# Kernel optimization log

Hardware: AMD Instinct MI355X
Metric: run time of the kernel (lower is better)

Reference implementation:

```python
import jax, jax.numpy as jnp
import numpy as np

HEADS = 16
DIM_HEAD = 64
SCALE = DIM_HEAD ** -0.5


def setup_inputs() -> dict:
    key = jax.random.key(0)
    k1, k2, k3, k4 = jax.random.split(key, 4)
    dim = 1024
    inner = HEADS * DIM_HEAD  # 1024
    b, n = 4, 2048
    x = jax.random.normal(k1, (b, n, dim), dtype=jnp.float32)
    # weights stored as [in, out] (equivalent math to torch Linear)
    w_qkv = jax.random.normal(k2, (dim, inner * 3), dtype=jnp.float32) * (dim ** -0.5)
    w_out = jax.random.normal(k3, (inner, dim), dtype=jnp.float32) * (inner ** -0.5)
    b_out = jax.random.normal(k4, (dim,), dtype=jnp.float32) * 0.01
    return {"x": x, "w_qkv": w_qkv, "w_out": w_out, "b_out": b_out}


def reference(x, w_qkv, w_out, b_out):
    b, n, dim = x.shape
    qkv = x @ w_qkv                                   # [b, n, 3*inner]
    q, k, v = jnp.split(qkv, 3, axis=-1)
    def to_heads(t):
        return t.reshape(b, n, HEADS, DIM_HEAD).transpose(0, 2, 1, 3)  # b h n d
    q, k, v = to_heads(q) * SCALE, to_heads(k), to_heads(v)
    dots = jnp.einsum('bhid,bhjd->bhij', q, k)        # [b, h, n, n]
    mask_value = -jnp.finfo(dots.dtype).max
    causal_mask = jnp.triu(jnp.ones((n, n), dtype=bool), k=1)
    dots = jnp.where(causal_mask, mask_value, dots)
    attn = jax.nn.softmax(dots, axis=-1)
    out = jnp.einsum('bhij,bhjd->bhid', attn, v)      # [b, h, n, d]
    out = out.transpose(0, 2, 1, 3).reshape(b, n, HEADS * DIM_HEAD)
    return out @ w_out + b_out
```

## Files before the change

### kernel.cpp

```cpp
#include <hip/hip_runtime.h>
#include <hip/hip_bf16.h>
#include <stdint.h>

typedef __attribute__((ext_vector_type(8))) short bf16x8;
typedef __attribute__((ext_vector_type(4))) float f32x4;
typedef __attribute__((ext_vector_type(4))) unsigned int uint32x4;

#define TOKENS 8192
#define DMODEL 1024
#define NQKV   3072
#define NSEQ   2048
#define NHEAD  16
#define DHEAD  64

__device__ __forceinline__ ushort f32_bf16(float f) {
    uint32_t u = __builtin_bit_cast(uint32_t, f);
    u = (u + 0x7fffu + ((u >> 16) & 1u)) >> 16;
    return (ushort)u;
}

__device__ __forceinline__ unsigned int cvt_pk_bf16(float lo, float hi) {
    unsigned int r;
    asm("v_cvt_pk_bf16_f32 %0, %1, %2" : "=v"(r) : "v"(lo), "v"(hi));
    return r;
}
__device__ __forceinline__ void permlane32_swap(unsigned int& a, unsigned int& b) {
    asm("v_permlane32_swap_b32 %0, %1" : "+v"(a), "+v"(b));
}
__device__ __forceinline__ void permlane16_swap(unsigned int& a, unsigned int& b) {
    asm("v_permlane16_swap_b32 %0, %1" : "+v"(a), "+v"(b));
}
__device__ __forceinline__ unsigned opaque_copy(unsigned x) {
    unsigned y;
    asm("v_mov_b32 %0, %1" : "=v"(y) : "v"(x));
    return y;
}

__device__ __forceinline__ float red_max_g(float x) {
    unsigned a = __builtin_bit_cast(unsigned, x);
    unsigned b = opaque_copy(a);
    permlane16_swap(a, b);
    float r = fmaxf(__builtin_bit_cast(float, a), __builtin_bit_cast(float, b));
    unsigned c = __builtin_bit_cast(unsigned, r);
    unsigned d = opaque_copy(c);
    permlane32_swap(c, d);
    return fmaxf(__builtin_bit_cast(float, c), __builtin_bit_cast(float, d));
}
__device__ __forceinline__ float red_sum_g(float x) {
    unsigned a = __builtin_bit_cast(unsigned, x);
    unsigned b = opaque_copy(a);
    permlane16_swap(a, b);
    float r = __builtin_bit_cast(float, a) + __builtin_bit_cast(float, b);
    unsigned c = __builtin_bit_cast(unsigned, r);
    unsigned d = opaque_copy(c);
    permlane32_swap(c, d);
    return __builtin_bit_cast(float, c) + __builtin_bit_cast(float, d);
}

__device__ __forceinline__ void gload16(const void* g, void* l) {
    __builtin_amdgcn_global_load_lds(
        (const __attribute__((address_space(1))) void*)g,
        (__attribute__((address_space(3))) void*)l, 16, 0, 0);
}

__global__ void cvt_x_kernel(const float* __restrict__ x, ushort* __restrict__ xb) {
    int i = blockIdx.x * 256 + threadIdx.x;
    float4 v = reinterpret_cast<const float4*>(x)[i];
    ushort4 o;
    o.x = f32_bf16(v.x); o.y = f32_bf16(v.y);
    o.z = f32_bf16(v.z); o.w = f32_bf16(v.w);
    reinterpret_cast<ushort4*>(xb)[i] = o;
}

__global__ __launch_bounds__(256) void cvt_wt_kernel(
    const float* __restrict__ w, ushort* __restrict__ wt, int N)
{
    __shared__ float tile[64][65];
    const int tid = threadIdx.x;
    const int r  = tid >> 4;
    const int c4 = (tid & 15) * 4;
    const int n0 = blockIdx.x * 64;
    const int k0 = blockIdx.y * 64;
    #pragma unroll
    for (int i = 0; i < 4; ++i) {
        const float4 v = *reinterpret_cast<const float4*>(&w[(size_t)(k0 + r + i * 16) * N + n0 + c4]);
        tile[r + i * 16][c4 + 0] = v.x;
        tile[r + i * 16][c4 + 1] = v.y;
        tile[r + i * 16][c4 + 2] = v.z;
        tile[r + i * 16][c4 + 3] = v.w;
    }
    __syncthreads();
    #pragma unroll
    for (int i = 0; i < 4; ++i) {
        ushort4 o;
        o.x = f32_bf16(tile[c4 + 0][r + i * 16]);
        o.y = f32_bf16(tile[c4 + 1][r + i * 16]);
        o.z = f32_bf16(tile[c4 + 2][r + i * 16]);
        o.w = f32_bf16(tile[c4 + 3][r + i * 16]);
        *reinterpret_cast<ushort4*>(&wt[(size_t)(n0 + r + i * 16) * 1024 + k0 + c4]) = o;
    }
}

__device__ __forceinline__ void barf() {
    asm volatile("" ::: "memory");
    __builtin_amdgcn_s_barrier();
    asm volatile("" ::: "memory");
}

template<int MODE>
__global__ __launch_bounds__(256) void gemm_bt(
    const ushort* __restrict__ A, const ushort* __restrict__ Bt,
    ushort* __restrict__ Qb, ushort* __restrict__ Kb, ushort* __restrict__ Vtb,
    float* __restrict__ Out, const float* __restrict__ bias)
{
    constexpr int K = 1024;
    __shared__ __align__(16) ushort As[2][128 * 32];
    __shared__ __align__(16) ushort Bs[2][128 * 32];

    const int lane = threadIdx.x & 63;
    const int w    = threadIdx.x >> 6;
    const int l16  = lane & 15;
    const int g    = lane >> 4;
    const int row0 = blockIdx.y * 128;
    const int col0 = blockIdx.x * 128;
    const int wr   = (w >> 1) * 64;
    const int wc   = (w & 1) * 64;

    const int srow  = w * 16 + (lane >> 2);
    const int sswz8 = ((lane & 3) ^ ((lane >> 3) & 3)) * 8;
    const ushort* Ag = A  + (size_t)(row0 + srow) * K + sswz8;
    const ushort* Bg = Bt + (size_t)(col0 + srow) * K + sswz8;
    const int woff = w * (16 * 32);

    const int cq8 = (g ^ ((l16 >> 1) & 3)) * 8;

    f32x4 acc[4][4] = {};

#define GSTAGE(BUF, KK) do {                                             \
        gload16(Ag + (KK),          &As[BUF][woff]);                     \
        gload16(Ag + 64 * K + (KK), &As[BUF][woff + 64 * 32]);           \
        gload16(Bg + (KK),          &Bs[BUF][woff]);                     \
        gload16(Bg + 64 * K + (KK), &Bs[BUF][woff + 64 * 32]);           \
    } while (0)

#define GCOMPUTE(BUF) do {                                               \
        bf16x8 a[4], b[4];                                               \
        _Pragma("unroll")                                                \
        for (int m = 0; m < 4; ++m)                                      \
            a[m] = *reinterpret_cast<const bf16x8*>(                     \
                &As[BUF][(wr + m * 16 + l16) * 32 + cq8]);               \
        _Pragma("unroll")                                                \
        for (int n = 0; n < 4; ++n)                                      \
            b[n] = *reinterpret_cast<const bf16x8*>(                     \
                &Bs[BUF][(wc + n * 16 + l16) * 32 + cq8]);               \
        _Pragma("unroll")                                                \
        for (int m = 0; m < 4; ++m)                                      \
            _Pragma("unroll")                                            \
            for (int n = 0; n < 4; ++n)                                  \
                acc[m][n] = __builtin_amdgcn_mfma_f32_16x16x32_bf16(     \
                    a[m], b[n], acc[m][n], 0, 0, 0);                     \
    } while (0)

    GSTAGE(0, 0);
    GSTAGE(1, 32);
    for (int kk = 0; kk + 128 <= K; kk += 64) {
        asm volatile("s_waitcnt vmcnt(4)" ::: "memory");
        barf();
        GCOMPUTE(0);
        barf();
        GSTAGE(0, kk + 64);
        asm volatile("s_waitcnt vmcnt(4)" ::: "memory");
        barf();
        GCOMPUTE(1);
        barf();
        GSTAGE(1, kk + 96);
    }
    asm volatile("s_waitcnt vmcnt(4)" ::: "memory");
    barf();
    GCOMPUTE(0);
    asm volatile("s_waitcnt vmcnt(0)" ::: "memory");
    barf();
    GCOMPUTE(1);
#undef GSTAGE
#undef GCOMPUTE

    if (MODE == 0) {
        const int part = col0 >> 10;
        const float QSC = 0.18033688011112042f;
        #pragma unroll
        for (int m = 0; m < 4; ++m) {
            const int trow = row0 + wr + m * 16 + 4 * g;
            #pragma unroll
            for (int n = 0; n < 4; ++n) {
                const int c  = col0 + wc + n * 16 + l16;
                const int cc = c & 1023;
                const int h  = cc >> 6, d = cc & 63;
                #pragma unroll
                for (int jj = 0; jj < 4; ++jj) {
                    const int t  = trow + jj;
                    const int bb = t >> 11, nn = t & 2047;
                    const float v = acc[m][n][jj];
                    const size_t bhid = (size_t)(bb * NHEAD + h);
                    if (part == 0)
                        Qb[(bhid * NSEQ + nn) * DHEAD + d] = f32_bf16(v * QSC);
                    else if (part == 1)
                        Kb[(bhid * NSEQ + nn) * DHEAD + d] = f32_bf16(v);
                    else
                        Vtb[bhid * (NSEQ * DHEAD) + (size_t)(nn >> 5) * (DHEAD * 32)
                            + d * 32 + (nn & 31)] = f32_bf16(v);
                }
            }
        }
    } else {
        #pragma unroll
        for (int m = 0; m < 4; ++m) {
            const int trow = row0 + wr + m * 16 + 4 * g;
            #pragma unroll
            for (int n = 0; n < 4; ++n) {
                const int c = col0 + wc + n * 16 + l16;
                const float bv = bias[c];
                #pragma unroll
                for (int jj = 0; jj < 4; ++jj)
                    Out[(size_t)(trow + jj) * DMODEL + c] = acc[m][n][jj] + bv;
            }
        }
    }
}

__device__ __forceinline__ void attn_qk(
    int kt, int qr0s, int l16, int g,
    const bf16x8 (&kk)[4][2],
    const bf16x8 qf0, const bf16x8 qf1,
    f32x4 (&oacc)[4], float& mrun, float& lsum,
    bf16x8& pf0, bf16x8& pf1)
{
    const f32x4 zero = {};
    f32x4 s[4];
    __builtin_amdgcn_s_setprio(1);
    #pragma unroll
    for (int t = 0; t < 4; ++t) {
        s[t] = __builtin_amdgcn_mfma_f32_16x16x32_bf16(kk[t][0], qf0, zero, 0, 0, 0);
        s[t] = __builtin_amdgcn_mfma_f32_16x16x32_bf16(kk[t][1], qf1, s[t], 0, 0, 0);
    }
    __builtin_amdgcn_s_setprio(0);
    if (kt + 63 > qr0s) {
        const int kb = kt + 4 * g - (qr0s + l16);
        #pragma unroll
        for (int t = 0; t < 4; ++t)
            #pragma unroll
            for (int jj = 0; jj < 4; ++jj)
                if (kb + 16 * t + jj > 0) s[t][jj] = -1e30f;
    }
    const float m0 = fmaxf(fmaxf(s[0][0], s[0][1]), s[0][2]);
    const float m1 = fmaxf(fmaxf(s[0][3], s[1][0]), s[1][1]);
    const float m2 = fmaxf(fmaxf(s[1][2], s[1][3]), s[2][0]);
    const float m3 = fmaxf(fmaxf(s[2][1], s[2][2]), s[2][3]);
    const float m4 = fmaxf(fmaxf(s[3][0], s[3][1]), s[3][2]);
    const float m5 = fmaxf(fmaxf(m0, m1), m2);
    const float m6 = fmaxf(fmaxf(m3, m4), s[3][3]);
    float mx = red_max_g(fmaxf(m5, m6));
    if (__any(mx > mrun + 8.0f)) {
        const float mn = fmaxf(mrun, mx);
        const float sc = __builtin_amdgcn_exp2f(mrun - mn);
        mrun = mn;
        lsum *= sc;
        float scj[4];
        #pragma unroll
        for (int jj = 0; jj < 4; ++jj) scj[jj] = __shfl(sc, 4 * g + jj);
        #pragma unroll
        for (int dt = 0; dt < 4; ++dt)
            #pragma unroll
            for (int jj = 0; jj < 4; ++jj) oacc[dt][jj] *= scj[jj];
    }
    float ps = 0.f;
    unsigned int pw[4][2];
    #pragma unroll
    for (int t = 0; t < 4; ++t) {
        const float p0 = __builtin_amdgcn_exp2f(s[t][0] - mrun);
        const float p1 = __builtin_amdgcn_exp2f(s[t][1] - mrun);
        const float p2 = __builtin_amdgcn_exp2f(s[t][2] - mrun);
        const float p3 = __builtin_amdgcn_exp2f(s[t][3] - mrun);
        ps += (p0 + p1) + (p2 + p3);
        pw[t][0] = cvt_pk_bf16(p0, p1);
        pw[t][1] = cvt_pk_bf16(p2, p3);
    }
    lsum += red_sum_g(ps);
    unsigned int a0 = pw[0][0], a1 = pw[0][1], b0 = pw[1][0], b1 = pw[1][1];
    permlane32_swap(a0, b0); permlane32_swap(a1, b1);
    permlane16_swap(a0, b0); permlane16_swap(a1, b1);
    pf0 = __builtin_bit_cast(bf16x8, (uint32x4){a0, a1, b0, b1});
    unsigned int c0 = pw[2][0], c1 = pw[2][1], d0 = pw[3][0], d1 = pw[3][1];
    permlane32_swap(c0, d0); permlane32_swap(c1, d1);
    permlane16_swap(c0, d0); permlane16_swap(c1, d1);
    pf1 = __builtin_bit_cast(bf16x8, (uint32x4){c0, c1, d0, d1});
}

__global__ __launch_bounds__(256) void attn_kernel(
    const ushort* __restrict__ Qb, const ushort* __restrict__ Kb,
    const ushort* __restrict__ Vt, ushort* __restrict__ Ob)
{
    __shared__ __align__(16) ushort Klds[2][4096];
    __shared__ __align__(16) ushort Vlds[2][4096];

    const int lane = threadIdx.x & 63;
    const int w    = threadIdx.x >> 6;
    const int l16  = lane & 15;
    const int g    = lane >> 4;

    const int bid = blockIdx.x;
    const int xcd = bid & 7, ii = bid >> 3;
    const int bh  = xcd * 8 + (ii >> 4);
    const int jlo = ii & 15;
    const int jhi = 31 - jlo;

    const int qr0_lo = jlo * 64 + w * 16;
    const int qr0_hi = jhi * 64 + w * 16;
    const int nt = jhi + 1;

    const ushort* QpL = Qb + ((size_t)bh * NSEQ + qr0_lo + l16) * DHEAD + 8 * g;
    const ushort* QpH = Qb + ((size_t)bh * NSEQ + qr0_hi + l16) * DHEAD + 8 * g;
    const bf16x8 qfL0 = *reinterpret_cast<const bf16x8*>(QpL);
    const bf16x8 qfL1 = *reinterpret_cast<const bf16x8*>(QpL + 32);
    const bf16x8 qfH0 = *reinterpret_cast<const bf16x8*>(QpH);
    const bf16x8 qfH1 = *reinterpret_cast<const bf16x8*>(QpH + 32);

    const ushort* Kg = Kb + (size_t)bh * (NSEQ * DHEAD);
    const ushort* Vg = Vt + (size_t)bh * (NSEQ * DHEAD);

    const int q0    = w * 2;
    const int srow  = lane >> 2;
    const int sswz8 = ((lane & 3) ^ ((lane >> 3) & 3)) * 8;
    const int cq8   = (g ^ ((l16 >> 1) & 3)) * 8;

    f32x4 oaccL[4] = {}, oaccH[4] = {};
    float mrunL = -1e30f, lsumL = 0.f, mrunH = -1e30f, lsumH = 0.f;

    #pragma unroll
    for (int i = 0; i < 2; ++i) {
        const int q = q0 + i;
        gload16(Kg + (size_t)((q & 3) * 16 + srow) * 64 + (q >> 2) * 32 + sswz8,
                &Klds[0][q * 512]);
        gload16(Vg + (size_t)(q >> 2) * 2048 + ((q & 3) * 16 + srow) * 32 + sswz8,
                &Vlds[0][q * 512]);
    }
    __syncthreads();

    for (int t = 0; t < nt; ++t) {
        const int cur = t & 1;
        if (t + 1 < nt) {
            const int kt1 = (t + 1) * 64;
            #pragma unroll
            for (int i = 0; i < 2; ++i) {
                const int q = q0 + i;
                gload16(Kg + (size_t)(kt1 + (q & 3) * 16 + srow) * 64 + (q >> 2) * 32 + sswz8,
                        &Klds[cur ^ 1][q * 512]);
                gload16(Vg + (size_t)kt1 * 64 + (q >> 2) * 2048 + ((q & 3) * 16 + srow) * 32 + sswz8,
                        &Vlds[cur ^ 1][q * 512]);
            }
        }
        const int kt = t * 64;
        bf16x8 kk[4][2];
        #pragma unroll
        for (int tt = 0; tt < 4; ++tt) {
            #pragma unroll
            for (int h = 0; h < 2; ++h)
                kk[tt][h] = *reinterpret_cast<const bf16x8*>(
                    &Klds[cur][h * 2048 + (16 * tt + l16) * 32 + cq8]);
        }
        bf16x8 pfH0, pfH1, pfL0, pfL1;
        attn_qk(kt, qr0_hi, l16, g, kk, qfH0, qfH1, oaccH, mrunH, lsumH, pfH0, pfH1);
        const bool doLo = (t <= jlo);
        if (doLo)
            attn_qk(kt, qr0_lo, l16, g, kk, qfL0, qfL1, oaccL, mrunL, lsumL, pfL0, pfL1);
        __builtin_amdgcn_s_setprio(1);
        #pragma unroll
        for (int dt = 0; dt < 4; ++dt) {
            const bf16x8 v0 = *reinterpret_cast<const bf16x8*>(
                &Vlds[cur][(dt * 16 + l16) * 32 + cq8]);
            const bf16x8 v1 = *reinterpret_cast<const bf16x8*>(
                &Vlds[cur][2048 + (dt * 16 + l16) * 32 + cq8]);
            oaccH[dt] = __builtin_amdgcn_mfma_f32_16x16x32_bf16(pfH0, v0, oaccH[dt], 0, 0, 0);
            oaccH[dt] = __builtin_amdgcn_mfma_f32_16x16x32_bf16(pfH1, v1, oaccH[dt], 0, 0, 0);
            if (doLo) {
                oaccL[dt] = __builtin_amdgcn_mfma_f32_16x16x32_bf16(pfL0, v0, oaccL[dt], 0, 0, 0);
                oaccL[dt] = __builtin_amdgcn_mfma_f32_16x16x32_bf16(pfL1, v1, oaccL[dt], 0, 0, 0);
            }
        }
        __builtin_amdgcn_s_setprio(0);
        __syncthreads();
    }

    const int bb = bh >> 4, h = bh & 15;
    {
        const float inv = 1.0f / lsumH;
        float invj[4];
        #pragma unroll
        for (int jj = 0; jj < 4; ++jj) invj[jj] = __shfl(inv, 4 * g + jj);
        #pragma unroll
        for (int jj = 0; jj < 4; ++jj) {
            const size_t t = (size_t)bb * NSEQ + qr0_hi + 4 * g + jj;
            #pragma unroll
            for (int dt = 0; dt < 4; ++dt)
                Ob[t * DMODEL + h * DHEAD + dt * 16 + l16] = f32_bf16(oaccH[dt][jj] * invj[jj]);
        }
    }
    {
        const float inv = 1.0f / lsumL;
        float invj[4];
        #pragma unroll
        for (int jj = 0; jj < 4; ++jj) invj[jj] = __shfl(inv, 4 * g + jj);
        #pragma unroll
        for (int jj = 0; jj < 4; ++jj) {
            const size_t t = (size_t)bb * NSEQ + qr0_lo + 4 * g + jj;
            #pragma unroll
            for (int dt = 0; dt < 4; ++dt)
                Ob[t * DMODEL + h * DHEAD + dt * 16 + l16] = f32_bf16(oaccL[dt][jj] * invj[jj]);
        }
    }
}

extern "C" void kernel_launch(void* const* d_in, const int* in_sizes, int n_in,
                              void* d_out, int out_size, void* d_ws, size_t ws_size,
                              hipStream_t stream)
{
    const float* x     = (const float*)d_in[0];
    const float* w_qkv = (const float*)d_in[1];
    const float* w_out = (const float*)d_in[2];
    const float* b_out = (const float*)d_in[3];
    float* out = (float*)d_out;

    char* ws = (char*)d_ws;
    ushort* x_bf   = (ushort*)(ws);
    ushort* wqkv_t = (ushort*)(ws + 16777216);
    ushort* wout_t = (ushort*)(ws + 23068672);
    ushort* q_bf   = (ushort*)(ws + 25165824);
    ushort* k_bf   = (ushort*)(ws + 41943040);
    ushort* vt_bf  = (ushort*)(ws + 58720256);
    ushort* attn_bf = x_bf;

    cvt_x_kernel<<<dim3(TOKENS * DMODEL / 4 / 256), dim3(256), 0, stream>>>(x, x_bf);
    cvt_wt_kernel<<<dim3(NQKV / 64, 1024 / 64), dim3(256), 0, stream>>>(w_qkv, wqkv_t, NQKV);
    cvt_wt_kernel<<<dim3(1024 / 64, 1024 / 64), dim3(256), 0, stream>>>(w_out, wout_t, 1024);

    gemm_bt<0><<<dim3(NQKV / 128, TOKENS / 128), dim3(256), 0, stream>>>(
        x_bf, wqkv_t, q_bf, k_bf, vt_bf, nullptr, nullptr);

    attn_kernel<<<dim3(1024), dim3(256), 0, stream>>>(q_bf, k_bf, vt_bf, attn_bf);

    gemm_bt<1><<<dim3(DMODEL / 128, TOKENS / 128), dim3(256), 0, stream>>>(
        attn_bf, wout_t, nullptr, nullptr, nullptr, out, b_out);
}
```

Baseline: 212.3 us.

## Use 256x256-tile, 4-stage pipelined GEMM with block swizzle for QKV projection

```diff
diff --git a/kernel.cpp b/kernel.cpp
--- a/kernel.cpp
+++ b/kernel.cpp
@@ -63,6 +63,12 @@
         (__attribute__((address_space(3))) void*)l, 16, 0, 0);
 }
 
+__device__ __forceinline__ void barf() {
+    asm volatile("" ::: "memory");
+    __builtin_amdgcn_s_barrier();
+    asm volatile("" ::: "memory");
+}
+
 __global__ void cvt_x_kernel(const float* __restrict__ x, ushort* __restrict__ xb) {
     int i = blockIdx.x * 256 + threadIdx.x;
     float4 v = reinterpret_cast<const float4*>(x)[i];
@@ -101,16 +107,116 @@
     }
 }
 
-__device__ __forceinline__ void barf() {
-    asm volatile("" ::: "memory");
-    __builtin_amdgcn_s_barrier();
-    asm volatile("" ::: "memory");
-}
-
-template<int MODE>
-__global__ __launch_bounds__(256) void gemm_bt(
+__global__ __launch_bounds__(512) void gemm256_qkv(
     const ushort* __restrict__ A, const ushort* __restrict__ Bt,
-    ushort* __restrict__ Qb, ushort* __restrict__ Kb, ushort* __restrict__ Vtb,
+    ushort* __restrict__ Qb, ushort* __restrict__ Kb, ushort* __restrict__ Vtb)
+{
+    constexpr int K  = 1024;
+    constexpr int NT = K / 32;
+    __shared__ __align__(16) ushort As[4][256 * 32];
+    __shared__ __align__(16) ushort Bs[4][256 * 32];
+
+    const int tid  = threadIdx.x;
+    const int lane = tid & 63;
+    const int w    = tid >> 6;
+    const int l16  = lane & 15;
+    const int g    = lane >> 4;
+
+    const int swz  = (blockIdx.x & 7) * 48 + (blockIdx.x >> 3);
+    const int row0 = (swz & 31) * 256;
+    const int col0 = (swz >> 5) * 256;
+
+    const int wrow = (w >> 2) * 128;
+    const int wcol = (w & 3) * 64;
+
+    const int sq8 = ((tid & 3) ^ ((tid >> 3) & 3)) * 8;
+    const ushort* Ag0 = A  + (size_t)(row0 + (tid >> 2)) * K + sq8;
+    const ushort* Ag1 = Ag0 + (size_t)128 * K;
+    const ushort* Bg0 = Bt + (size_t)(col0 + (tid >> 2)) * K + sq8;
+    const ushort* Bg1 = Bg0 + (size_t)128 * K;
+    const int dst0 = w * 16 * 32;
+    const int dst1 = (128 + w * 16) * 32;
+
+    const int cq8 = (g ^ ((l16 >> 1) & 3)) * 8;
+
+    f32x4 acc[8][4] = {};
+
+#define STAGE256(T) do { const int _b = (T) & 3; const size_t _k = (size_t)(T) * 32; \
+        gload16(Ag0 + _k, &As[_b][dst0]);                                  \
+        gload16(Ag1 + _k, &As[_b][dst1]);                                  \
+        gload16(Bg0 + _k, &Bs[_b][dst0]);                                  \
+        gload16(Bg1 + _k, &Bs[_b][dst1]);                                  \
+    } while (0)
+
+    STAGE256(0); STAGE256(1); STAGE256(2);
+
+    for (int t = 0; t < NT; ++t) {
+        const int buf = t & 3;
+        if (t < NT - 2)       asm volatile("s_waitcnt vmcnt(8)" ::: "memory");
+        else if (t == NT - 2) asm volatile("s_waitcnt vmcnt(4)" ::: "memory");
+        else                  asm volatile("s_waitcnt vmcnt(0)" ::: "memory");
+        barf();
+        bf16x8 a[4], b[4];
+        #pragma unroll
+        for (int n = 0; n < 4; ++n)
+            b[n] = *reinterpret_cast<const bf16x8*>(
+                &Bs[buf][(wcol + n * 16 + l16) * 32 + cq8]);
+        #pragma unroll
+        for (int m = 0; m < 4; ++m)
+            a[m] = *reinterpret_cast<const bf16x8*>(
+                &As[buf][(wrow + m * 16 + l16) * 32 + cq8]);
+        if (t + 3 < NT) STAGE256(t + 3);
+        __builtin_amdgcn_s_setprio(1);
+        #pragma unroll
+        for (int m = 0; m < 4; ++m)
+            #pragma unroll
+            for (int n = 0; n < 4; ++n)
+                acc[m][n] = __builtin_amdgcn_mfma_f32_16x16x32_bf16(a[m], b[n], acc[m][n], 0, 0, 0);
+        __builtin_amdgcn_s_setprio(0);
+        #pragma unroll
+        for (int m = 0; m < 4; ++m)
+            a[m] = *reinterpret_cast<const bf16x8*>(
+                &As[buf][(wrow + 64 + m * 16 + l16) * 32 + cq8]);
+        __builtin_amdgcn_s_setprio(1);
+        #pragma unroll
+        for (int m = 0; m < 4; ++m)
+            #pragma unroll
+            for (int n = 0; n < 4; ++n)
+                acc[4 + m][n] = __builtin_amdgcn_mfma_f32_16x16x32_bf16(a[m], b[n], acc[4 + m][n], 0, 0, 0);
+        __builtin_amdgcn_s_setprio(0);
+    }
+#undef STAGE256
+
+    const float QSC = 0.18033688011112042f;
+    const int part = col0 >> 10;
+    #pragma unroll
+    for (int m = 0; m < 8; ++m) {
+        const int trow = row0 + wrow + m * 16 + 4 * g;
+        #pragma unroll
+        for (int n = 0; n < 4; ++n) {
+            const int c  = col0 + wcol + n * 16 + l16;
+            const int cc = c & 1023;
+            const int h  = cc >> 6, d = cc & 63;
+            #pragma unroll
+            for (int jj = 0; jj < 4; ++jj) {
+                const int t  = trow + jj;
+                const int bb = t >> 11, nn = t & 2047;
+                const float v = acc[m][n][jj];
+                const size_t bhid = (size_t)(bb * NHEAD + h);
+                if (part == 0)
+                    Qb[(bhid * NSEQ + nn) * DHEAD + d] = f32_bf16(v * QSC);
+                else if (part == 1)
+                    Kb[(bhid * NSEQ + nn) * DHEAD + d] = f32_bf16(v);
+                else
+                    Vtb[bhid * (NSEQ * DHEAD) + (size_t)(nn >> 5) * (DHEAD * 32)
+                        + d * 32 + (nn & 31)] = f32_bf16(v);
+            }
+        }
+    }
+}
+
+__global__ __launch_bounds__(256) void gemm_out(
+    const ushort* __restrict__ A, const ushort* __restrict__ Bt,
     float* __restrict__ Out, const float* __restrict__ bias)
 {
     constexpr int K = 1024;
@@ -131,7 +237,6 @@
     const ushort* Ag = A  + (size_t)(row0 + srow) * K + sswz8;
     const ushort* Bg = Bt + (size_t)(col0 + srow) * K + sswz8;
     const int woff = w * (16 * 32);
-
     const int cq8 = (g ^ ((l16 >> 1) & 3)) * 8;
 
     f32x4 acc[4][4] = {};
@@ -142,7 +247,6 @@
         gload16(Bg + (KK),          &Bs[BUF][woff]);                     \
         gload16(Bg + 64 * K + (KK), &Bs[BUF][woff + 64 * 32]);           \
     } while (0)
-
 #define GCOMPUTE(BUF) do {                                               \
         bf16x8 a[4], b[4];                                               \
         _Pragma("unroll")                                                \
@@ -184,45 +288,16 @@
 #undef GSTAGE
 #undef GCOMPUTE
 
-    if (MODE == 0) {
-        const int part = col0 >> 10;
-        const float QSC = 0.18033688011112042f;
-        #pragma unroll
-        for (int m = 0; m < 4; ++m) {
-            const int trow = row0 + wr + m * 16 + 4 * g;
-            #pragma unroll
-            for (int n = 0; n < 4; ++n) {
-                const int c  = col0 + wc + n * 16 + l16;
-                const int cc = c & 1023;
-                const int h  = cc >> 6, d = cc & 63;
-                #pragma unroll
-                for (int jj = 0; jj < 4; ++jj) {
-                    const int t  = trow + jj;
-                    const int bb = t >> 11, nn = t & 2047;
-                    const float v = acc[m][n][jj];
-                    const size_t bhid = (size_t)(bb * NHEAD + h);
-                    if (part == 0)
-                        Qb[(bhid * NSEQ + nn) * DHEAD + d] = f32_bf16(v * QSC);
-                    else if (part == 1)
-                        Kb[(bhid * NSEQ + nn) * DHEAD + d] = f32_bf16(v);
-                    else
-                        Vtb[bhid * (NSEQ * DHEAD) + (size_t)(nn >> 5) * (DHEAD * 32)
-                            + d * 32 + (nn & 31)] = f32_bf16(v);
-                }
-            }
-        }
-    } else {
-        #pragma unroll
-        for (int m = 0; m < 4; ++m) {
-            const int trow = row0 + wr + m * 16 + 4 * g;
-            #pragma unroll
-            for (int n = 0; n < 4; ++n) {
-                const int c = col0 + wc + n * 16 + l16;
-                const float bv = bias[c];
-                #pragma unroll
-                for (int jj = 0; jj < 4; ++jj)
-                    Out[(size_t)(trow + jj) * DMODEL + c] = acc[m][n][jj] + bv;
-            }
+    #pragma unroll
+    for (int m = 0; m < 4; ++m) {
+        const int trow = row0 + wr + m * 16 + 4 * g;
+        #pragma unroll
+        for (int n = 0; n < 4; ++n) {
+            const int c = col0 + wc + n * 16 + l16;
+            const float bv = bias[c];
+            #pragma unroll
+            for (int jj = 0; jj < 4; ++jj)
+                Out[(size_t)(trow + jj) * DMODEL + c] = acc[m][n][jj] + bv;
         }
     }
 }
@@ -442,11 +517,11 @@
     cvt_wt_kernel<<<dim3(NQKV / 64, 1024 / 64), dim3(256), 0, stream>>>(w_qkv, wqkv_t, NQKV);
     cvt_wt_kernel<<<dim3(1024 / 64, 1024 / 64), dim3(256), 0, stream>>>(w_out, wout_t, 1024);
 
-    gemm_bt<0><<<dim3(NQKV / 128, TOKENS / 128), dim3(256), 0, stream>>>(
-        x_bf, wqkv_t, q_bf, k_bf, vt_bf, nullptr, nullptr);
+    gemm256_qkv<<<dim3((TOKENS / 256) * (NQKV / 256)), dim3(512), 0, stream>>>(
+        x_bf, wqkv_t, q_bf, k_bf, vt_bf);
 
     attn_kernel<<<dim3(1024), dim3(256), 0, stream>>>(q_bf, k_bf, vt_bf, attn_bf);
 
-    gemm_bt<1><<<dim3(DMODEL / 128, TOKENS / 128), dim3(256), 0, stream>>>(
-        attn_bf, wout_t, nullptr, nullptr, nullptr, out, b_out);
-}
+    gemm_out<<<dim3(DMODEL / 128, TOKENS / 128), dim3(256), 0, stream>>>(
+        attn_bf, wout_t, out, b_out);
+}
```

New measurement: 244.5 us. +15.2%, slower.
